# Optimization experiments

Hardware: AMD Instinct MI355X
Metric: run time of the kernel (lower is better)

The kernel has to match this reference:

```python
import jax, jax.numpy as jnp
import numpy as np

M, N, WIDTH, DEPTH = 32768, 4096, 128, 4
KSCALE = 0.02  # keep kernel@act in tanh's active range


def setup_inputs() -> dict:
    key = jax.random.key(0)
    ks = jax.random.split(key, 6)
    act = jax.random.normal(ks[0], (M, WIDTH), dtype=jnp.float32)
    self_act = jax.random.normal(ks[1], (N, WIDTH), dtype=jnp.float32)
    kernel = jax.random.normal(ks[2], (M, N), dtype=jnp.float32) * KSCALE
    self_kernel = jax.random.normal(ks[3], (N, N), dtype=jnp.float32) * KSCALE
    # per-depth params from hk.layer_stack: glorot-uniform weights, zero bias
    limit = np.sqrt(6.0 / (WIDTH + WIDTH))
    weights = jax.random.uniform(ks[4], (DEPTH, WIDTH, WIDTH), dtype=jnp.float32,
                                 minval=-limit, maxval=limit)
    bias = jnp.zeros((DEPTH, WIDTH), dtype=jnp.float32)
    return {"act": act, "self_act": self_act, "kernel": kernel,
            "self_kernel": self_kernel, "weights": weights, "bias": bias}


def reference(act, self_act, kernel, self_kernel, weights, bias):
    # One depth step (shared W,b used for both branches, as in ScatteringLayer
    # instantiated once per scattering_fn):
    #   act      += tanh((kernel @ self_act) @ W.T + b)        [M, width]
    #   self_act += tanh((self_kernel @ self_act) @ W.T + b)   [N, width]
    # (deterministic=True -> dropout is a no-op; safe_key=None requires it)
    def step(carry, params):
        a, s = carry
        W, b = params
        msg = jnp.einsum('mn,nk->mk', kernel, s)        # kernel message pass
        self_msg = jnp.einsum('nm,mk->nk', self_kernel, s)
        a = a + jnp.tanh(jnp.einsum('mk,ik->mi', msg, W) + b)
        s = s + jnp.tanh(jnp.einsum('nk,ik->ni', self_msg, W) + b)
        return (a, s), None

    (act_out, self_act_out), _ = jax.lax.scan(step, (act, self_act), (weights, bias))
    return act_out, self_act_out
```

## Files before the change

### kernel.cpp

```cpp
#include <hip/hip_runtime.h>

#define M_SZ 32768
#define N_SZ 4096
#define DEPTHS 4
#define SPLITK 8
#define KCH 512

typedef __attribute__((ext_vector_type(8))) short bh8;
typedef __attribute__((ext_vector_type(4))) float f4;
typedef unsigned short u16;
typedef unsigned int u32;

#define SBAR() __builtin_amdgcn_s_barrier()
#define FENCE() asm volatile("" ::: "memory")
#define WAITV(n) asm volatile("s_waitcnt vmcnt(" #n ")" ::: "memory")
#define WAITVL(n) asm volatile("s_waitcnt vmcnt(" #n ") lgkmcnt(0)" ::: "memory")

__device__ __forceinline__ u16 f2bf(float f) {
  u32 u = __float_as_uint(f);
  u = (u + 0x7FFFu + ((u >> 16) & 1u)) >> 16;
  return (u16)u;
}

__device__ __forceinline__ float fast_tanh(float x) {
  float ax = __builtin_fabsf(x);
  float e = __builtin_exp2f(ax * 2.8853900817779268f);
  float r = 1.0f - 2.0f * __builtin_amdgcn_rcpf(e + 1.0f);
  return __builtin_copysignf(r, x);
}

__device__ __forceinline__ void async16(const void* g, void* l) {
  __builtin_amdgcn_global_load_lds((const __attribute__((address_space(1))) u32*)g,
                                   (__attribute__((address_space(3))) u32*)l, 16, 0, 0);
}

__global__ void k1_kernel(const float* __restrict__ s, const float* __restrict__ Wd,
                          u16* __restrict__ Ytd) {
  const int n = blockIdx.x * 256 + threadIdx.x;
  const int i0 = blockIdx.y * 8;
  float acc[8] = {0.f, 0.f, 0.f, 0.f, 0.f, 0.f, 0.f, 0.f};
  const float4* srow = (const float4*)(s + (size_t)n * 128);
#pragma unroll 4
  for (int k4 = 0; k4 < 32; ++k4) {
    float4 sv = srow[k4];
#pragma unroll
    for (int ii = 0; ii < 8; ++ii) {
      const float* w = Wd + (i0 + ii) * 128 + k4 * 4;
      acc[ii] = fmaf(sv.x, w[0], acc[ii]);
      acc[ii] = fmaf(sv.y, w[1], acc[ii]);
      acc[ii] = fmaf(sv.z, w[2], acc[ii]);
      acc[ii] = fmaf(sv.w, w[3], acc[ii]);
    }
  }
#pragma unroll
  for (int ii = 0; ii < 8; ++ii)
    Ytd[(size_t)(i0 + ii) * 4096 + n] = f2bf(acc[ii]);
}

__global__ __launch_bounds__(512, 2) void k2a_kernel(
    const float* __restrict__ SK, const u16* __restrict__ Ytd, float* __restrict__ Zp) {
  __shared__ char smem[8192 + 2 * 8192];
  char* sA = smem;
  char* sB0 = smem + 8192;
  char* sB1 = smem + 8192 + 8192;
  const int t = threadIdx.x, lane = t & 63, wid = t >> 6;
  const int wr = wid >> 2, wc = wid & 3;
  const int n0 = blockIdx.x * 128;
  const int kbase = blockIdx.y * KCH;

  const int arow = t >> 2, kseg = t & 3;
  const float4* ag = (const float4*)(SK + (size_t)(n0 + arow) * 4096 + kbase + kseg * 8);
  const int awoff = arow * 64 + ((kseg ^ (arow & 3)) << 4);

  const int P = wid * 64 + lane;
  const int bcol = P >> 2;
  const int bg = (P & 3) ^ (bcol & 3);
  const u16* bsrc = Ytd + (size_t)bcol * 4096 + kbase + bg * 8;
  const int bldst = wid * 1024;

  const int l15 = lane & 15, l4 = lane >> 4;
  int aro[4], bro[2];
#pragma unroll
  for (int mf = 0; mf < 4; ++mf) {
    int row = wr * 64 + mf * 16 + l15;
    aro[mf] = row * 64 + ((l4 ^ (row & 3)) << 4);
  }
#pragma unroll
  for (int n2 = 0; n2 < 2; ++n2) {
    int col = wc * 32 + n2 * 16 + l15;
    bro[n2] = col * 64 + ((l4 ^ (col & 3)) << 4);
  }

  f4 acc[4][2];
#pragma unroll
  for (int i = 0; i < 4; ++i)
#pragma unroll
    for (int j = 0; j < 2; ++j) acc[i][j] = (f4){0.f, 0.f, 0.f, 0.f};

  float4 va0 = ag[0], va1 = ag[1];
  FENCE();
  async16(bsrc, sB0 + bldst);
  FENCE();

  char* sBc = sB0;
  char* sBn = sB1;
  for (int k = 0; k < 15; ++k) {
    SBAR(); FENCE();
    WAITV(1);
    union { bh8 v; u16 u[8]; } p;
    p.u[0] = f2bf(va0.x); p.u[1] = f2bf(va0.y); p.u[2] = f2bf(va0.z); p.u[3] = f2bf(va0.w);
    p.u[4] = f2bf(va1.x); p.u[5] = f2bf(va1.y); p.u[6] = f2bf(va1.z); p.u[7] = f2bf(va1.w);
    *(bh8*)(sA + awoff) = p.v;
    FENCE();
    va0 = ag[(k + 1) * 8]; va1 = ag[(k + 1) * 8 + 1];
    FENCE();
    WAITVL(2);
    SBAR(); FENCE();
    async16(bsrc + (k + 1) * 32, sBn + bldst);
    FENCE();
    bh8 af[4];
#pragma unroll
    for (int mf = 0; mf < 4; ++mf) af[mf] = *(const bh8*)(sA + aro[mf]);
#pragma unroll
    for (int n2 = 0; n2 < 2; ++n2) {
      bh8 b = *(const bh8*)(sBc + bro[n2]);
#pragma unroll
      for (int mf = 0; mf < 4; ++mf)
        acc[mf][n2] = __builtin_amdgcn_mfma_f32_16x16x32_bf16(af[mf], b, acc[mf][n2], 0, 0, 0);
    }
    char* tp = sBc; sBc = sBn; sBn = tp;
  }
  SBAR(); FENCE();
  WAITV(1);
  {
    union { bh8 v; u16 u[8]; } p;
    p.u[0] = f2bf(va0.x); p.u[1] = f2bf(va0.y); p.u[2] = f2bf(va0.z); p.u[3] = f2bf(va0.w);
    p.u[4] = f2bf(va1.x); p.u[5] = f2bf(va1.y); p.u[6] = f2bf(va1.z); p.u[7] = f2bf(va1.w);
    *(bh8*)(sA + awoff) = p.v;
  }
  WAITVL(0);
  SBAR(); FENCE();
  {
    bh8 af[4];
#pragma unroll
    for (int mf = 0; mf < 4; ++mf) af[mf] = *(const bh8*)(sA + aro[mf]);
#pragma unroll
    for (int n2 = 0; n2 < 2; ++n2) {
      bh8 b = *(const bh8*)(sBc + bro[n2]);
#pragma unroll
      for (int mf = 0; mf < 4; ++mf)
        acc[mf][n2] = __builtin_amdgcn_mfma_f32_16x16x32_bf16(af[mf], b, acc[mf][n2], 0, 0, 0);
    }
  }

  float* Z = Zp + (size_t)blockIdx.y * (N_SZ * 128) + (size_t)n0 * 128;
#pragma unroll
  for (int mf = 0; mf < 4; ++mf)
#pragma unroll
    for (int n2 = 0; n2 < 2; ++n2)
#pragma unroll
      for (int q = 0; q < 4; ++q) {
        int r = wr * 64 + mf * 16 + l4 * 4 + q;
        int c = wc * 32 + n2 * 16 + l15;
        Z[r * 128 + c] = acc[mf][n2][q];
      }
}

__global__ void k2b_kernel(float* __restrict__ s, const float* __restrict__ Zp,
                           const float* __restrict__ bd) {
  int idx = blockIdx.x * 256 + threadIdx.x;
  float v = bd[idx & 127];
#pragma unroll
  for (int c = 0; c < SPLITK; ++c) v += Zp[(size_t)c * (N_SZ * 128) + idx];
  s[idx] += fast_tanh(v);
}

__global__ __launch_bounds__(1024, 4) void pB_kernel(
    const float* __restrict__ A, const u16* __restrict__ Yt,
    const float* __restrict__ act, const float* __restrict__ bias,
    float* __restrict__ outA) {
  __shared__ char smem[8192 + 2 * 32768];
  char* sA = smem;
  char* sB0 = smem + 8192;
  char* sB1 = smem + 8192 + 32768;
  const int t = threadIdx.x, lane = t & 63, wid = t >> 6;
  const int wr = wid >> 3, wc = wid & 7;
  const int m0 = blockIdx.x * 128;
  const int l15 = lane & 15, l4 = lane >> 4;

  const int arow = t >> 3, aseg = t & 7;
  const float4* agp = (const float4*)(A + (size_t)(m0 + arow) * 4096 + aseg * 4);
  const int awoff = arow * 64 + (((aseg >> 1) ^ (arow & 3)) << 4) + ((aseg & 1) << 3);

  const u16* bsrc[2];
  int bldst[2];
#pragma unroll
  for (int j = 0; j < 2; ++j) {
    int G = j * 1024 + t;
    int col = G >> 2;
    int g = (G & 3) ^ (col & 3);
    bsrc[j] = Yt + (size_t)col * 4096 + g * 8;
    bldst[j] = (j * 16 + wid) * 1024;
  }

  int aro[4], bro[4];
#pragma unroll
  for (int mf = 0; mf < 4; ++mf) {
    int row = wr * 64 + mf * 16 + l15;
    aro[mf] = row * 64 + ((l4 ^ (row & 3)) << 4);
  }
#pragma unroll
  for (int d = 0; d < 4; ++d) {
    int tc = d * 128 + wc * 16 + l15;
    bro[d] = tc * 64 + ((l4 ^ (tc & 3)) << 4);
  }

  f4 acc[4][4];
#pragma unroll
  for (int i = 0; i < 4; ++i)
#pragma unroll
    for (int j = 0; j < 4; ++j) acc[i][j] = (f4){0.f, 0.f, 0.f, 0.f};

  float4 va = agp[0];
  FENCE();
  async16(bsrc[0], sB0 + bldst[0]);
  async16(bsrc[1], sB0 + bldst[1]);
  FENCE();

  char* sBc = sB0;
  char* sBn = sB1;
#pragma unroll 1
  for (int k = 0; k < 127; ++k) {
    SBAR(); FENCE();
    WAITV(2);
    union { uint2 v; u16 u[4]; } p;
    p.u[0] = f2bf(va.x); p.u[1] = f2bf(va.y); p.u[2] = f2bf(va.z); p.u[3] = f2bf(va.w);
    *(uint2*)(sA + awoff) = p.v;
    FENCE();
    va = agp[(k + 1) * 8];
    FENCE();
    WAITVL(1);
    SBAR(); FENCE();
    async16(bsrc[0] + (k + 1) * 32, sBn + bldst[0]);
    async16(bsrc[1] + (k + 1) * 32, sBn + bldst[1]);
    FENCE();
    bh8 af[4];
#pragma unroll
    for (int mf = 0; mf < 4; ++mf) af[mf] = *(const bh8*)(sA + aro[mf]);
#pragma unroll
    for (int d = 0; d < 4; ++d) {
      bh8 b = *(const bh8*)(sBc + bro[d]);
#pragma unroll
      for (int mf = 0; mf < 4; ++mf)
        acc[mf][d] = __builtin_amdgcn_mfma_f32_16x16x32_bf16(af[mf], b, acc[mf][d], 0, 0, 0);
    }
    char* tp = sBc; sBc = sBn; sBn = tp;
  }
  SBAR(); FENCE();
  WAITV(2);
  {
    union { uint2 v; u16 u[4]; } p;
    p.u[0] = f2bf(va.x); p.u[1] = f2bf(va.y); p.u[2] = f2bf(va.z); p.u[3] = f2bf(va.w);
    *(uint2*)(sA + awoff) = p.v;
  }
  WAITVL(0);
  SBAR(); FENCE();
  {
    bh8 af[4];
#pragma unroll
    for (int mf = 0; mf < 4; ++mf) af[mf] = *(const bh8*)(sA + aro[mf]);
#pragma unroll
    for (int d = 0; d < 4; ++d) {
      bh8 b = *(const bh8*)(sBc + bro[d]);
#pragma unroll
      for (int mf = 0; mf < 4; ++mf)
        acc[mf][d] = __builtin_amdgcn_mfma_f32_16x16x32_bf16(af[mf], b, acc[mf][d], 0, 0, 0);
    }
  }

  float bsv[4];
#pragma unroll
  for (int d = 0; d < 4; ++d) bsv[d] = bias[d * 128 + wc * 16 + l15];
#pragma unroll
  for (int mf = 0; mf < 4; ++mf)
#pragma unroll
    for (int q = 0; q < 4; ++q) {
      int r = m0 + wr * 64 + mf * 16 + l4 * 4 + q;
      int c = wc * 16 + l15;
      float s = 0.f;
#pragma unroll
      for (int d = 0; d < 4; ++d) s += fast_tanh(acc[mf][d][q] + bsv[d]);
      size_t o = (size_t)r * 128 + c;
      outA[o] = act[o] + s;
    }
}

extern "C" void kernel_launch(void* const* d_in, const int* in_sizes, int n_in,
                              void* d_out, int out_size, void* d_ws, size_t ws_size,
                              hipStream_t stream) {
  const float* act = (const float*)d_in[0];
  const float* self_act = (const float*)d_in[1];
  const float* kern = (const float*)d_in[2];
  const float* self_kern = (const float*)d_in[3];
  const float* weights = (const float*)d_in[4];
  const float* bias = (const float*)d_in[5];
  float* out = (float*)d_out;
  float* s_buf = out + (size_t)M_SZ * 128;

  char* ws = (char*)d_ws;
  u16* Yt = (u16*)ws;
  float* Zp = (float*)(ws + (4u << 20));

  hipMemcpyAsync(s_buf, self_act, (size_t)N_SZ * 128 * sizeof(float),
                 hipMemcpyDeviceToDevice, stream);

  for (int d = 0; d < DEPTHS; ++d) {
    k1_kernel<<<dim3(16, 16), 256, 0, stream>>>(s_buf, weights + d * 16384,
                                                Yt + (size_t)d * 128 * 4096);
    k2a_kernel<<<dim3(32, SPLITK), 512, 0, stream>>>(self_kern,
                                                     Yt + (size_t)d * 128 * 4096, Zp);
    k2b_kernel<<<2048, 256, 0, stream>>>(s_buf, Zp, bias + d * 128);
  }
  pB_kernel<<<256, 1024, 0, stream>>>(kern, Yt, act, bias, out);
}
```

Measured before the change: 371.3 us.

## Fuse split-K reduction into k2a via last-block atomic counter; drop initial memcpy

Removes the separate k2b reduction kernel by having the last split-K block per row tile (detected with an atomic counter reset in k1) sum the partials, add bias, apply tanh and update self_act. Also removes the initial device-to-device copy by reading self_act directly at depth 0 and writing into the output buffer. This cuts four kernel launches and one copy. In exchange, the reduction now runs in only 32 blocks, which serializes that work onto a few CUs, and correctness depends on threadfence ordering.

```diff
diff --git a/kernel.cpp b/kernel.cpp
--- a/kernel.cpp
+++ b/kernel.cpp
@@ -35,8 +35,10 @@
 }
 
 __global__ void k1_kernel(const float* __restrict__ s, const float* __restrict__ Wd,
-                          u16* __restrict__ Ytd) {
-  const int n = blockIdx.x * 256 + threadIdx.x;
+                          u16* __restrict__ Ytd, u32* __restrict__ cnt) {
+  const int t = threadIdx.x;
+  if (blockIdx.x == 0 && blockIdx.y == 0 && t < 32) cnt[t] = 0;
+  const int n = blockIdx.x * 256 + t;
   const int i0 = blockIdx.y * 8;
   float acc[8] = {0.f, 0.f, 0.f, 0.f, 0.f, 0.f, 0.f, 0.f};
   const float4* srow = (const float4*)(s + (size_t)n * 128);
@@ -58,8 +60,11 @@
 }
 
 __global__ __launch_bounds__(512, 2) void k2a_kernel(
-    const float* __restrict__ SK, const u16* __restrict__ Ytd, float* __restrict__ Zp) {
+    const float* __restrict__ SK, const u16* __restrict__ Ytd, float* __restrict__ Zp,
+    const float* __restrict__ s_src, float* __restrict__ s_out,
+    const float* __restrict__ bd, u32* __restrict__ cnt) {
   __shared__ char smem[8192 + 2 * 8192];
+  __shared__ u32 lastFlag;
   char* sA = smem;
   char* sB0 = smem + 8192;
   char* sB1 = smem + 8192 + 8192;
@@ -164,15 +169,22 @@
         int c = wc * 32 + n2 * 16 + l15;
         Z[r * 128 + c] = acc[mf][n2][q];
       }
-}
-
-__global__ void k2b_kernel(float* __restrict__ s, const float* __restrict__ Zp,
-                           const float* __restrict__ bd) {
-  int idx = blockIdx.x * 256 + threadIdx.x;
-  float v = bd[idx & 127];
-#pragma unroll
-  for (int c = 0; c < SPLITK; ++c) v += Zp[(size_t)c * (N_SZ * 128) + idx];
-  s[idx] += fast_tanh(v);
+
+  __threadfence();
+  __syncthreads();
+  if (t == 0) lastFlag = (atomicAdd(&cnt[blockIdx.x], 1) == SPLITK - 1) ? 1u : 0u;
+  __syncthreads();
+  if (lastFlag) {
+    __threadfence();
+    for (int idx = t; idx < 128 * 128; idx += 512) {
+      int r = idx >> 7, ccol = idx & 127;
+      size_t gi = (size_t)(n0 + r) * 128 + ccol;
+      float v = bd[ccol];
+#pragma unroll
+      for (int cc = 0; cc < SPLITK; ++cc) v += Zp[(size_t)cc * (N_SZ * 128) + gi];
+      s_out[gi] = s_src[gi] + fast_tanh(v);
+    }
+  }
 }
 
 __global__ __launch_bounds__(1024, 4) void pB_kernel(
@@ -310,16 +322,16 @@
   char* ws = (char*)d_ws;
   u16* Yt = (u16*)ws;
   float* Zp = (float*)(ws + (4u << 20));
-
-  hipMemcpyAsync(s_buf, self_act, (size_t)N_SZ * 128 * sizeof(float),
-                 hipMemcpyDeviceToDevice, stream);
+  u32* counters = (u32*)(ws + (20u << 20));
 
   for (int d = 0; d < DEPTHS; ++d) {
-    k1_kernel<<<dim3(16, 16), 256, 0, stream>>>(s_buf, weights + d * 16384,
-                                                Yt + (size_t)d * 128 * 4096);
+    const float* s_src = (d == 0) ? self_act : s_buf;
+    k1_kernel<<<dim3(16, 16), 256, 0, stream>>>(s_src, weights + d * 16384,
+                                                Yt + (size_t)d * 128 * 4096, counters);
     k2a_kernel<<<dim3(32, SPLITK), 512, 0, stream>>>(self_kern,
-                                                     Yt + (size_t)d * 128 * 4096, Zp);
-    k2b_kernel<<<2048, 256, 0, stream>>>(s_buf, Zp, bias + d * 128);
+                                                     Yt + (size_t)d * 128 * 4096, Zp,
+                                                     s_src, s_buf, bias + d * 128,
+                                                     counters);
   }
   pB_kernel<<<256, 1024, 0, stream>>>(kern, Yt, act, bias, out);
 }
```

Measured after the change: 661.1 us. 1.78x slower.

## Retile self-kernel GEMM to 64-row tiles with 64-wide K steps, drop init memcpy

Applied to the files above, without the earlier changes.

The k2a split-K GEMM now uses 64-row blocks (twice the grid) with a 64-element K step per iteration and an 8-way XOR swizzle, doubling B staging to two async loads per thread and halving loop iterations. Occupancy hint is raised to 4 blocks per CU. The initial device-to-device copy of self_act is removed by having the first depth read self_act directly and k2b write out-of-place. This aims to improve parallelism and cut per-iteration sync overhead, at the cost of re-reading Ytd more often across more blocks.

```diff
diff --git a/kernel.cpp b/kernel.cpp
--- a/kernel.cpp
+++ b/kernel.cpp
@@ -57,81 +57,82 @@
     Ytd[(size_t)(i0 + ii) * 4096 + n] = f2bf(acc[ii]);
 }
 
-__global__ __launch_bounds__(512, 2) void k2a_kernel(
+__global__ __launch_bounds__(512, 4) void k2a_kernel(
     const float* __restrict__ SK, const u16* __restrict__ Ytd, float* __restrict__ Zp) {
-  __shared__ char smem[8192 + 2 * 8192];
+  __shared__ char smem[8192 + 2 * 16384];
   char* sA = smem;
   char* sB0 = smem + 8192;
-  char* sB1 = smem + 8192 + 8192;
+  char* sB1 = smem + 8192 + 16384;
   const int t = threadIdx.x, lane = t & 63, wid = t >> 6;
-  const int wr = wid >> 2, wc = wid & 3;
-  const int n0 = blockIdx.x * 128;
-  const int kbase = blockIdx.y * KCH;
-
-  const int arow = t >> 2, kseg = t & 3;
-  const float4* ag = (const float4*)(SK + (size_t)(n0 + arow) * 4096 + kbase + kseg * 8);
-  const int awoff = arow * 64 + ((kseg ^ (arow & 3)) << 4);
-
-  const int P = wid * 64 + lane;
-  const int bcol = P >> 2;
-  const int bg = (P & 3) ^ (bcol & 3);
-  const u16* bsrc = Ytd + (size_t)bcol * 4096 + kbase + bg * 8;
-  const int bldst = wid * 1024;
-
+  const int nb = blockIdx.x, c = blockIdx.y;
+  const int n0 = nb * 64;
+  const int kbz = c * KCH;
+  const int wr = wid >> 1, wc = wid & 1;
   const int l15 = lane & 15, l4 = lane >> 4;
-  int aro[4], bro[2];
-#pragma unroll
-  for (int mf = 0; mf < 4; ++mf) {
-    int row = wr * 64 + mf * 16 + l15;
-    aro[mf] = row * 64 + ((l4 ^ (row & 3)) << 4);
-  }
-#pragma unroll
-  for (int n2 = 0; n2 < 2; ++n2) {
-    int col = wc * 32 + n2 * 16 + l15;
-    bro[n2] = col * 64 + ((l4 ^ (col & 3)) << 4);
-  }
-
-  f4 acc[4][2];
-#pragma unroll
-  for (int i = 0; i < 4; ++i)
-#pragma unroll
-    for (int j = 0; j < 2; ++j) acc[i][j] = (f4){0.f, 0.f, 0.f, 0.f};
-
-  float4 va0 = ag[0], va1 = ag[1];
+
+  const int arow = t >> 3, kseg8 = t & 7;
+  const float4* agz = (const float4*)(SK + (size_t)(n0 + arow) * 4096 + kbz + kseg8 * 8);
+  const int awoff = arow * 128 + ((kseg8 ^ (arow & 7)) << 4);
+
+  int bcol[2], bgq[2], bldst[2];
+#pragma unroll
+  for (int j = 0; j < 2; ++j) {
+    int G = j * 512 + t;
+    bcol[j] = G >> 3;
+    bgq[j] = (G & 7) ^ (bcol[j] & 7);
+    bldst[j] = G * 16;
+  }
+
+  int aro, bro[4];
+  {
+    int row = wr * 16 + l15;
+    aro = row * 128 + ((l4 ^ (row & 7)) << 4);
+  }
+#pragma unroll
+  for (int n2 = 0; n2 < 4; ++n2) {
+    int col = wc * 64 + n2 * 16 + l15;
+    bro[n2] = col * 128 + ((l4 ^ (col & 7)) << 4);
+  }
+
+  f4 acc[4];
+#pragma unroll
+  for (int j = 0; j < 4; ++j) acc[j] = (f4){0.f, 0.f, 0.f, 0.f};
+
+  float4 va0 = agz[0], va1 = agz[1];
   FENCE();
-  async16(bsrc, sB0 + bldst);
+  async16(Ytd + (size_t)bcol[0] * 4096 + kbz + bgq[0] * 8, sB0 + bldst[0]);
+  async16(Ytd + (size_t)bcol[1] * 4096 + kbz + bgq[1] * 8, sB0 + bldst[1]);
   FENCE();
-
   char* sBc = sB0;
   char* sBn = sB1;
-  for (int k = 0; k < 15; ++k) {
+  for (int k = 0; k < 7; ++k) {
     SBAR(); FENCE();
-    WAITV(1);
+    WAITV(2);
     union { bh8 v; u16 u[8]; } p;
     p.u[0] = f2bf(va0.x); p.u[1] = f2bf(va0.y); p.u[2] = f2bf(va0.z); p.u[3] = f2bf(va0.w);
     p.u[4] = f2bf(va1.x); p.u[5] = f2bf(va1.y); p.u[6] = f2bf(va1.z); p.u[7] = f2bf(va1.w);
     *(bh8*)(sA + awoff) = p.v;
     FENCE();
-    va0 = ag[(k + 1) * 8]; va1 = ag[(k + 1) * 8 + 1];
+    va0 = agz[(k + 1) * 16]; va1 = agz[(k + 1) * 16 + 1];
     FENCE();
     WAITVL(2);
     SBAR(); FENCE();
-    async16(bsrc + (k + 1) * 32, sBn + bldst);
-    FENCE();
-    bh8 af[4];
-#pragma unroll
-    for (int mf = 0; mf < 4; ++mf) af[mf] = *(const bh8*)(sA + aro[mf]);
-#pragma unroll
-    for (int n2 = 0; n2 < 2; ++n2) {
-      bh8 b = *(const bh8*)(sBc + bro[n2]);
-#pragma unroll
-      for (int mf = 0; mf < 4; ++mf)
-        acc[mf][n2] = __builtin_amdgcn_mfma_f32_16x16x32_bf16(af[mf], b, acc[mf][n2], 0, 0, 0);
+    async16(Ytd + (size_t)bcol[0] * 4096 + kbz + bgq[0] * 8 + (k + 1) * 64, sBn + bldst[0]);
+    async16(Ytd + (size_t)bcol[1] * 4096 + kbz + bgq[1] * 8 + (k + 1) * 64, sBn + bldst[1]);
+    FENCE();
+#pragma unroll
+    for (int kk = 0; kk < 2; ++kk) {
+      bh8 a = *(const bh8*)(sA + (aro ^ (kk << 6)));
+#pragma unroll
+      for (int n2 = 0; n2 < 4; ++n2) {
+        bh8 bb = *(const bh8*)(sBc + (bro[n2] ^ (kk << 6)));
+        acc[n2] = __builtin_amdgcn_mfma_f32_16x16x32_bf16(a, bb, acc[n2], 0, 0, 0);
+      }
     }
     char* tp = sBc; sBc = sBn; sBn = tp;
   }
   SBAR(); FENCE();
-  WAITV(1);
+  WAITV(2);
   {
     union { bh8 v; u16 u[8]; } p;
     p.u[0] = f2bf(va0.x); p.u[1] = f2bf(va0.y); p.u[2] = f2bf(va0.z); p.u[3] = f2bf(va0.w);
@@ -140,39 +141,34 @@
   }
   WAITVL(0);
   SBAR(); FENCE();
-  {
-    bh8 af[4];
-#pragma unroll
-    for (int mf = 0; mf < 4; ++mf) af[mf] = *(const bh8*)(sA + aro[mf]);
-#pragma unroll
-    for (int n2 = 0; n2 < 2; ++n2) {
-      bh8 b = *(const bh8*)(sBc + bro[n2]);
-#pragma unroll
-      for (int mf = 0; mf < 4; ++mf)
-        acc[mf][n2] = __builtin_amdgcn_mfma_f32_16x16x32_bf16(af[mf], b, acc[mf][n2], 0, 0, 0);
-    }
-  }
-
-  float* Z = Zp + (size_t)blockIdx.y * (N_SZ * 128) + (size_t)n0 * 128;
-#pragma unroll
-  for (int mf = 0; mf < 4; ++mf)
-#pragma unroll
-    for (int n2 = 0; n2 < 2; ++n2)
-#pragma unroll
-      for (int q = 0; q < 4; ++q) {
-        int r = wr * 64 + mf * 16 + l4 * 4 + q;
-        int c = wc * 32 + n2 * 16 + l15;
-        Z[r * 128 + c] = acc[mf][n2][q];
-      }
-}
-
-__global__ void k2b_kernel(float* __restrict__ s, const float* __restrict__ Zp,
-                           const float* __restrict__ bd) {
+#pragma unroll
+  for (int kk = 0; kk < 2; ++kk) {
+    bh8 a = *(const bh8*)(sA + (aro ^ (kk << 6)));
+#pragma unroll
+    for (int n2 = 0; n2 < 4; ++n2) {
+      bh8 bb = *(const bh8*)(sBc + (bro[n2] ^ (kk << 6)));
+      acc[n2] = __builtin_amdgcn_mfma_f32_16x16x32_bf16(a, bb, acc[n2], 0, 0, 0);
+    }
+  }
+
+  float* Z = Zp + (size_t)c * (N_SZ * 128) + (size_t)n0 * 128;
+#pragma unroll
+  for (int n2 = 0; n2 < 4; ++n2)
+#pragma unroll
+    for (int q = 0; q < 4; ++q) {
+      int r = wr * 16 + l4 * 4 + q;
+      int cc = wc * 64 + n2 * 16 + l15;
+      Z[r * 128 + cc] = acc[n2][q];
+    }
+}
+
+__global__ void k2b_kernel(const float* __restrict__ s_src, float* __restrict__ s_dst,
+                           const float* __restrict__ Zp, const float* __restrict__ bd) {
   int idx = blockIdx.x * 256 + threadIdx.x;
   float v = bd[idx & 127];
 #pragma unroll
   for (int c = 0; c < SPLITK; ++c) v += Zp[(size_t)c * (N_SZ * 128) + idx];
-  s[idx] += fast_tanh(v);
+  s_dst[idx] = s_src[idx] + fast_tanh(v);
 }
 
 __global__ __launch_bounds__(1024, 4) void pB_kernel(
@@ -311,15 +307,13 @@
   u16* Yt = (u16*)ws;
   float* Zp = (float*)(ws + (4u << 20));
 
-  hipMemcpyAsync(s_buf, self_act, (size_t)N_SZ * 128 * sizeof(float),
-                 hipMemcpyDeviceToDevice, stream);
-
   for (int d = 0; d < DEPTHS; ++d) {
-    k1_kernel<<<dim3(16, 16), 256, 0, stream>>>(s_buf, weights + d * 16384,
+    const float* s_src = (d == 0) ? self_act : s_buf;
+    k1_kernel<<<dim3(16, 16), 256, 0, stream>>>(s_src, weights + d * 16384,
                                                 Yt + (size_t)d * 128 * 4096);
-    k2a_kernel<<<dim3(32, SPLITK), 512, 0, stream>>>(self_kern,
+    k2a_kernel<<<dim3(64, SPLITK), 512, 0, stream>>>(self_kern,
                                                      Yt + (size_t)d * 128 * 4096, Zp);
-    k2b_kernel<<<2048, 256, 0, stream>>>(s_buf, Zp, bias + d * 128);
+    k2b_kernel<<<2048, 256, 0, stream>>>(s_src, s_buf, Zp, bias + d * 128);
   }
   pB_kernel<<<256, 1024, 0, stream>>>(kern, Yt, act, bias, out);
 }
```

Result: no change. 365.9 us (-1.5%).
